# Kernel tuning notes

Hardware: AMD Instinct MI355X
Metric: run time of the kernel (lower is better)

## Reference

```python
import jax, jax.numpy as jnp
import numpy as np

H = 8   # no_heads
D = 32  # c_hidden per head


def setup_inputs() -> dict:
    key = jax.random.key(0)
    ks = jax.random.split(key, 8)
    B, Q, K, C = 4, 1024, 1024, 256
    s = 0.02
    return {
        "q_x": jax.random.normal(ks[0], (B, Q, C), jnp.float32),
        "kv_x": jax.random.normal(ks[1], (B, K, C), jnp.float32),
        "mask_bias": jnp.zeros((B, 1, 1, K), jnp.float32),
        "pair_bias": jax.random.normal(ks[2], (B, H, Q, K), jnp.float32),
        "wq": jax.random.normal(ks[3], (H * D, C), jnp.float32) * s,
        "wk": jax.random.normal(ks[4], (H * D, C), jnp.float32) * s,
        "wv": jax.random.normal(ks[5], (H * D, C), jnp.float32) * s,
        "wg": jax.random.normal(ks[6], (H * D, C), jnp.float32) * s,
        "bg": jnp.zeros((H * D,), jnp.float32),
        "wo": jax.random.normal(ks[7], (C, H * D), jnp.float32) * s,
        "bo": jnp.zeros((C,), jnp.float32),
    }


def reference(q_x, kv_x, mask_bias, pair_bias, wq, wk, wv, wg, bg, wo, bo):
    B, Q, _ = q_x.shape
    K = kv_x.shape[1]
    # linear projections (no bias on q/k/v, as in OpenFold Attention)
    q = (q_x @ wq.T).reshape(B, Q, H, D) / jnp.sqrt(jnp.asarray(D, q_x.dtype))
    k = (kv_x @ wk.T).reshape(B, K, H, D)
    v = (kv_x @ wv.T).reshape(B, K, H, D)
    # scores + biases (mask bias broadcasts over heads/queries)
    a = jnp.einsum("bqhd,bkhd->bhqk", q, k) + mask_bias + pair_bias
    a = jax.nn.softmax(a, axis=-1)
    o = jnp.einsum("bhqk,bkhd->bqhd", a, v)  # [B,Q,H,D]
    # multiplicative gating from the query input
    g = jax.nn.sigmoid(q_x @ wg.T + bg).reshape(B, Q, H, D)
    o = o * g
    return (o.reshape(B, Q, H * D)) @ wo.T + bo
```

## Files before the change

kernel.cpp:

```cpp
#include <hip/hip_runtime.h>
#include <cstdint>
#include <cstddef>

typedef short bf16x8 __attribute__((ext_vector_type(8)));
typedef float f32x4 __attribute__((ext_vector_type(4)));
typedef unsigned short u16x4 __attribute__((ext_vector_type(4)));
typedef unsigned short u16x8 __attribute__((ext_vector_type(8)));

#define MFMA(a,b,c) __builtin_amdgcn_mfma_f32_16x16x32_bf16((a),(b),(c),0,0,0)

__device__ __forceinline__ unsigned short f2bf(float x){
  union { float f; unsigned u; } v; v.f = x;
  unsigned r = v.u + 0x7FFFu + ((v.u >> 16) & 1u);
  return (unsigned short)(r >> 16);
}
__device__ __forceinline__ float bf2f(unsigned short b){
  union { unsigned u; float f; } v; v.u = ((unsigned)b) << 16;
  return v.f;
}
__device__ __forceinline__ bf16x8 cvtld8(const float* p){
  f32x4 a = *(const f32x4*)p;
  f32x4 b = *(const f32x4*)(p + 4);
  bf16x8 r;
  r[0]=(short)f2bf(a.x); r[1]=(short)f2bf(a.y);
  r[2]=(short)f2bf(a.z); r[3]=(short)f2bf(a.w);
  r[4]=(short)f2bf(b.x); r[5]=(short)f2bf(b.y);
  r[6]=(short)f2bf(b.z); r[7]=(short)f2bf(b.w);
  return r;
}

__global__ __launch_bounds__(256) void wcvt_kernel(
    const float* __restrict__ wq, const float* __restrict__ wk,
    const float* __restrict__ wv, const float* __restrict__ wg,
    const float* __restrict__ wo, unsigned short* __restrict__ dst)
{
  const int which = blockIdx.x >> 5;
  const float* s = (which==0)?wq:(which==1)?wk:(which==2)?wv:(which==3)?wg:wo;
  const int off = (blockIdx.x & 31) * 2048 + threadIdx.x * 8;
  f32x4 a = *(const f32x4*)(s + off);
  f32x4 b = *(const f32x4*)(s + off + 4);
  u16x8 r;
  r[0]=f2bf(a.x); r[1]=f2bf(a.y); r[2]=f2bf(a.z); r[3]=f2bf(a.w);
  r[4]=f2bf(b.x); r[5]=f2bf(b.y); r[6]=f2bf(b.z); r[7]=f2bf(b.w);
  *(u16x8*)(dst + (size_t)which*65536 + off) = r;
}

__global__ __launch_bounds__(256,2) void proj_kernel(
    const float* __restrict__ q_x, const float* __restrict__ kv_x,
    const unsigned short* __restrict__ wb,
    const float* __restrict__ bg,
    unsigned short* __restrict__ qws, unsigned short* __restrict__ kws,
    unsigned short* __restrict__ vTws, unsigned short* __restrict__ gws)
{
  const int tid = threadIdx.x;
  const int w = tid >> 6, lane = tid & 63;
  const int c = lane & 15, qd = lane >> 4;
  const int side = blockIdx.x >> 8;
  const int rb = (blockIdx.x & 255) * 16;
  const float* X = side ? kv_x : q_x;
  const unsigned short* W0 = wb + (size_t)(side ? 1 : 0) * 65536;
  const unsigned short* W1 = wb + (size_t)(side ? 2 : 3) * 65536;
  const int hdw = w * 64;

  const f32x4 fz = {0.f,0.f,0.f,0.f};
  f32x4 acc[2][4];
  #pragma unroll
  for (int o=0;o<2;o++)
    #pragma unroll
    for (int mt=0;mt<4;mt++) acc[o][mt] = fz;

  #pragma unroll
  for (int ks = 0; ks < 8; ks++){
    const int ko = ks*32 + qd*8;
    bf16x8 bfrag = cvtld8(X + (size_t)(rb + c)*256 + ko);
    #pragma unroll
    for (int mt = 0; mt < 4; mt++){
      const int hd = hdw + mt*16 + c;
      bf16x8 a0 = *(const bf16x8*)(W0 + (size_t)hd*256 + ko);
      bf16x8 a1 = *(const bf16x8*)(W1 + (size_t)hd*256 + ko);
      acc[0][mt] = MFMA(a0, bfrag, acc[0][mt]);
      acc[1][mt] = MFMA(a1, bfrag, acc[1][mt]);
    }
  }

  const int row = rb + c;
  const int b = row >> 10, rr = row & 1023;
  #pragma unroll
  for (int mt = 0; mt < 4; mt++){
    const int hd0 = hdw + mt*16 + qd*4;
    const int h = hd0 >> 5, d0 = hd0 & 31;
    f32x4 v0 = acc[0][mt], v1 = acc[1][mt];
    if (side == 0){
      const float qs = 0.17677669529663687f;
      u16x4 oq = { f2bf(v0.x*qs), f2bf(v0.y*qs), f2bf(v0.z*qs), f2bf(v0.w*qs) };
      *(u16x4*)(qws + ((size_t)((b*8 + h)*1024 + rr))*32 + d0) = oq;
      f32x4 bg4 = *(const f32x4*)(bg + hd0);
      float g0 = 1.f/(1.f + exp2f(-1.44269504f*(v1.x + bg4.x)));
      float g1 = 1.f/(1.f + exp2f(-1.44269504f*(v1.y + bg4.y)));
      float g2 = 1.f/(1.f + exp2f(-1.44269504f*(v1.z + bg4.z)));
      float g3 = 1.f/(1.f + exp2f(-1.44269504f*(v1.w + bg4.w)));
      u16x4 og = { f2bf(g0), f2bf(g1), f2bf(g2), f2bf(g3) };
      *(u16x4*)(gws + ((size_t)((b*1024 + rr)*8 + h))*32 + d0) = og;
    } else {
      u16x4 ok = { f2bf(v0.x), f2bf(v0.y), f2bf(v0.z), f2bf(v0.w) };
      *(u16x4*)(kws + ((size_t)((b*8 + h)*1024 + rr))*32 + d0) = ok;
      size_t vb = ((size_t)((b*8 + h)*32 + d0))*1024 + rr;
      vTws[vb         ] = f2bf(v1.x);
      vTws[vb + 1024  ] = f2bf(v1.y);
      vTws[vb + 2048  ] = f2bf(v1.z);
      vTws[vb + 3072  ] = f2bf(v1.w);
    }
  }
}

__global__ __launch_bounds__(256,2) void attn_kernel(
    const float* __restrict__ pair_bias, const float* __restrict__ mask_bias,
    const unsigned short* __restrict__ qws, const unsigned short* __restrict__ kws,
    const unsigned short* __restrict__ vTws, const unsigned short* __restrict__ gws,
    unsigned short* __restrict__ ows)
{
  __shared__ __align__(16) unsigned char smem[67072];
  unsigned short* kT = (unsigned short*)smem;
  unsigned short* vT = (unsigned short*)(smem + 16384);
  unsigned short* pT = (unsigned short*)(smem + 33280);

  const int tid = threadIdx.x;
  const int w = tid >> 6, lane = tid & 63;
  const int c = lane & 15, qd = lane >> 4;
  const int bh = blockIdx.x >> 4, qb = blockIdx.x & 15;
  const int b  = bh >> 3, h = bh & 7;
  const int qrow = qb*64 + w*16 + c;

  const bf16x8 qf = *(const bf16x8*)(qws + ((size_t)bh*1024 + qrow)*32 + qd*8);
  const float* pbp = pair_bias + ((size_t)bh*1024 + qrow)*1024;
  const float* mbp = mask_bias + (size_t)b*1024;
  unsigned short* pTw = pT + w*4224;

  const f32x4 fz = {0.f,0.f,0.f,0.f};
  float m_i = -3.0e38f, l_i = 0.f;
  f32x4 accO0 = fz, accO1 = fz;

  for (int kc = 0; kc < 4; kc++){
    const int k0 = kc*256;
    #pragma unroll
    for (int i = 0; i < 4; i++){
      const int idx = i*256 + tid;
      const int plane = idx >> 8, key = idx & 255;
      u16x8 t8 = *(const u16x8*)(kws + ((size_t)bh*1024 + k0 + key)*32 + plane*8);
      *(u16x8*)(kT + idx*8) = t8;
    }
    #pragma unroll
    for (int i = 0; i < 4; i++){
      const int idx = i*256 + tid;
      const int d = idx >> 5, kch = idx & 31;
      u16x8 t8 = *(const u16x8*)(vTws + ((size_t)bh*32 + d)*1024 + k0 + kch*8);
      *(u16x8*)(vT + d*264 + kch*8) = t8;
    }
    __syncthreads();

    f32x4 sf[16];
    float cmax = -3.0e38f;
    #pragma unroll
    for (int t = 0; t < 16; t++){
      bf16x8 af = *(const bf16x8*)(kT + (qd*256 + t*16 + c)*8);
      f32x4 s = MFMA(af, qf, fz);
      f32x4 pb = *(const f32x4*)(pbp + k0 + t*16 + qd*4);
      f32x4 mb = *(const f32x4*)(mbp + k0 + t*16 + qd*4);
      s = (s + pb + mb) * 1.44269504f;
      sf[t] = s;
      cmax = fmaxf(cmax, fmaxf(fmaxf(s.x, s.y), fmaxf(s.z, s.w)));
    }
    cmax = fmaxf(cmax, __shfl_xor(cmax, 16));
    cmax = fmaxf(cmax, __shfl_xor(cmax, 32));
    const float m_new = fmaxf(m_i, cmax);
    const float alpha = exp2f(m_i - m_new);
    accO0 *= alpha; accO1 *= alpha;

    float rsum = 0.f;
    #pragma unroll
    for (int t = 0; t < 16; t++){
      f32x4 p;
      p.x = exp2f(sf[t].x - m_new);
      p.y = exp2f(sf[t].y - m_new);
      p.z = exp2f(sf[t].z - m_new);
      p.w = exp2f(sf[t].w - m_new);
      rsum += (p.x + p.y) + (p.z + p.w);
      u16x4 pk = { f2bf(p.x), f2bf(p.y), f2bf(p.z), f2bf(p.w) };
      *(u16x4*)(pTw + c*264 + t*16 + qd*4) = pk;
    }
    rsum += __shfl_xor(rsum, 16);
    rsum += __shfl_xor(rsum, 32);
    l_i = l_i*alpha + rsum;
    m_i = m_new;

    #pragma unroll
    for (int ks = 0; ks < 8; ks++){
      bf16x8 pf = *(const bf16x8*)(pTw + c*264 + ks*32 + qd*8);
      bf16x8 v0 = *(const bf16x8*)(vT + c*264 + ks*32 + qd*8);
      bf16x8 v1 = *(const bf16x8*)(vT + (16 + c)*264 + ks*32 + qd*8);
      accO0 = MFMA(v0, pf, accO0);
      accO1 = MFMA(v1, pf, accO1);
    }
    __syncthreads();
  }

  const float inv_l = 1.0f / l_i;
  const size_t obase = (((size_t)b*1024 + qrow)*8 + h)*32;
  {
    u16x4 g4 = *(const u16x4*)(gws + obase + qd*4);
    u16x4 o4 = { f2bf(accO0.x*inv_l*bf2f(g4[0])),
                 f2bf(accO0.y*inv_l*bf2f(g4[1])),
                 f2bf(accO0.z*inv_l*bf2f(g4[2])),
                 f2bf(accO0.w*inv_l*bf2f(g4[3])) };
    *(u16x4*)(ows + obase + qd*4) = o4;
  }
  {
    u16x4 g4 = *(const u16x4*)(gws + obase + 16 + qd*4);
    u16x4 o4 = { f2bf(accO1.x*inv_l*bf2f(g4[0])),
                 f2bf(accO1.y*inv_l*bf2f(g4[1])),
                 f2bf(accO1.z*inv_l*bf2f(g4[2])),
                 f2bf(accO1.w*inv_l*bf2f(g4[3])) };
    *(u16x4*)(ows + obase + 16 + qd*4) = o4;
  }
}

__global__ __launch_bounds__(256,2) void oproj_kernel(
    const unsigned short* __restrict__ ows, const unsigned short* __restrict__ wob,
    const float* __restrict__ bo, float* __restrict__ out)
{
  const int tid = threadIdx.x;
  const int w = tid >> 6, lane = tid & 63;
  const int c = lane & 15, qd = lane >> 4;
  const int row0 = blockIdx.x * 16;
  const int i0 = w * 64;

  const f32x4 fz = {0.f,0.f,0.f,0.f};
  f32x4 acc[4] = {fz, fz, fz, fz};
  #pragma unroll
  for (int ks = 0; ks < 8; ks++){
    const int ko = ks*32 + qd*8;
    bf16x8 bfrag = *(const bf16x8*)(ows + (size_t)(row0 + c)*256 + ko);
    #pragma unroll
    for (int mt = 0; mt < 4; mt++){
      bf16x8 afrag = *(const bf16x8*)(wob + (size_t)(i0 + mt*16 + c)*256 + ko);
      acc[mt] = MFMA(afrag, bfrag, acc[mt]);
    }
  }
  #pragma unroll
  for (int mt = 0; mt < 4; mt++){
    const int i = i0 + mt*16 + qd*4;
    f32x4 bo4 = *(const f32x4*)(bo + i);
    f32x4 r = acc[mt] + bo4;
    *(f32x4*)(out + (size_t)(row0 + c)*256 + i) = r;
  }
}

extern "C" void kernel_launch(void* const* d_in, const int* in_sizes, int n_in,
                              void* d_out, int out_size, void* d_ws, size_t ws_size,
                              hipStream_t stream) {
  const float* q_x       = (const float*)d_in[0];
  const float* kv_x      = (const float*)d_in[1];
  const float* mask_bias = (const float*)d_in[2];
  const float* pair_bias = (const float*)d_in[3];
  const float* wq        = (const float*)d_in[4];
  const float* wk        = (const float*)d_in[5];
  const float* wv        = (const float*)d_in[6];
  const float* wg        = (const float*)d_in[7];
  const float* bg        = (const float*)d_in[8];
  const float* wo        = (const float*)d_in[9];
  const float* bo        = (const float*)d_in[10];

  unsigned short* ws  = (unsigned short*)d_ws;
  unsigned short* qws  = ws;
  unsigned short* kws  = ws + (1u<<20);
  unsigned short* vTws = ws + 2*(1u<<20);
  unsigned short* gws  = ws + 3*(1u<<20);
  unsigned short* ows  = ws + 4*(1u<<20);
  unsigned short* wb   = ws + 5*(1u<<20);

  wcvt_kernel<<<160, 256, 0, stream>>>(wq, wk, wv, wg, wo, wb);
  proj_kernel<<<512, 256, 0, stream>>>(q_x, kv_x, wb, bg, qws, kws, vTws, gws);
  attn_kernel<<<512, 256, 0, stream>>>(pair_bias, mask_bias, qws, kws, vTws, gws, ows);
  oproj_kernel<<<256, 256, 0, stream>>>(ows, wb + 4*65536, bo, (float*)d_out);
}
```

Baseline: 254.3 us.

## Read K/V fragments directly from global memory, drop LDS staging and block barriers

The attention kernel stops staging K and V^T tiles in shared memory and instead loads the MFMA operand fragments straight from global memory (relying on L1/L2 reuse across the four waves). The key chunk shrinks from 256 to 128, which shrinks the per-wave P buffer, and the two __syncthreads per chunk are removed. Launch bounds are raised to allow four blocks per SIMD group for higher occupancy. The trade-off is redundant global/L2 traffic for K/V, since each wave now fetches the same fragments, in exchange for less LDS use, no barriers, and more waves to hide the dominant pair_bias streaming latency.

Result: slower. 268.5 us (+5.6%).

```diff
diff --git a/kernel.cpp b/kernel.cpp
--- a/kernel.cpp
+++ b/kernel.cpp
@@ -113,16 +113,13 @@
   }
 }
 
-__global__ __launch_bounds__(256,2) void attn_kernel(
+__global__ __launch_bounds__(256,4) void attn_kernel(
     const float* __restrict__ pair_bias, const float* __restrict__ mask_bias,
     const unsigned short* __restrict__ qws, const unsigned short* __restrict__ kws,
     const unsigned short* __restrict__ vTws, const unsigned short* __restrict__ gws,
     unsigned short* __restrict__ ows)
 {
-  __shared__ __align__(16) unsigned char smem[67072];
-  unsigned short* kT = (unsigned short*)smem;
-  unsigned short* vT = (unsigned short*)(smem + 16384);
-  unsigned short* pT = (unsigned short*)(smem + 33280);
+  __shared__ __align__(16) unsigned short pT[4*16*136];
 
   const int tid = threadIdx.x;
   const int w = tid >> 6, lane = tid & 63;
@@ -134,38 +131,25 @@
   const bf16x8 qf = *(const bf16x8*)(qws + ((size_t)bh*1024 + qrow)*32 + qd*8);
   const float* pbp = pair_bias + ((size_t)bh*1024 + qrow)*1024;
   const float* mbp = mask_bias + (size_t)b*1024;
-  unsigned short* pTw = pT + w*4224;
+  const unsigned short* kbase = kws  + (size_t)bh*1024*32;
+  const unsigned short* vbase = vTws + (size_t)bh*32*1024;
+  unsigned short* pTw = pT + w*(16*136);
 
   const f32x4 fz = {0.f,0.f,0.f,0.f};
   float m_i = -3.0e38f, l_i = 0.f;
   f32x4 accO0 = fz, accO1 = fz;
 
-  for (int kc = 0; kc < 4; kc++){
-    const int k0 = kc*256;
-    #pragma unroll
-    for (int i = 0; i < 4; i++){
-      const int idx = i*256 + tid;
-      const int plane = idx >> 8, key = idx & 255;
-      u16x8 t8 = *(const u16x8*)(kws + ((size_t)bh*1024 + k0 + key)*32 + plane*8);
-      *(u16x8*)(kT + idx*8) = t8;
-    }
-    #pragma unroll
-    for (int i = 0; i < 4; i++){
-      const int idx = i*256 + tid;
-      const int d = idx >> 5, kch = idx & 31;
-      u16x8 t8 = *(const u16x8*)(vTws + ((size_t)bh*32 + d)*1024 + k0 + kch*8);
-      *(u16x8*)(vT + d*264 + kch*8) = t8;
-    }
-    __syncthreads();
-
-    f32x4 sf[16];
+  for (int kc = 0; kc < 8; kc++){
+    const int k0 = kc*128;
+    f32x4 sf[8];
     float cmax = -3.0e38f;
     #pragma unroll
-    for (int t = 0; t < 16; t++){
-      bf16x8 af = *(const bf16x8*)(kT + (qd*256 + t*16 + c)*8);
+    for (int t = 0; t < 8; t++){
+      const int kt = k0 + t*16;
+      bf16x8 af = *(const bf16x8*)(kbase + (size_t)(kt + c)*32 + qd*8);
       f32x4 s = MFMA(af, qf, fz);
-      f32x4 pb = *(const f32x4*)(pbp + k0 + t*16 + qd*4);
-      f32x4 mb = *(const f32x4*)(mbp + k0 + t*16 + qd*4);
+      f32x4 pb = *(const f32x4*)(pbp + kt + qd*4);
+      f32x4 mb = *(const f32x4*)(mbp + kt + qd*4);
       s = (s + pb + mb) * 1.44269504f;
       sf[t] = s;
       cmax = fmaxf(cmax, fmaxf(fmaxf(s.x, s.y), fmaxf(s.z, s.w)));
@@ -178,7 +162,7 @@
 
     float rsum = 0.f;
     #pragma unroll
-    for (int t = 0; t < 16; t++){
+    for (int t = 0; t < 8; t++){
       f32x4 p;
       p.x = exp2f(sf[t].x - m_new);
       p.y = exp2f(sf[t].y - m_new);
@@ -186,7 +170,7 @@
       p.w = exp2f(sf[t].w - m_new);
       rsum += (p.x + p.y) + (p.z + p.w);
       u16x4 pk = { f2bf(p.x), f2bf(p.y), f2bf(p.z), f2bf(p.w) };
-      *(u16x4*)(pTw + c*264 + t*16 + qd*4) = pk;
+      *(u16x4*)(pTw + c*136 + t*16 + qd*4) = pk;
     }
     rsum += __shfl_xor(rsum, 16);
     rsum += __shfl_xor(rsum, 32);
@@ -194,14 +178,13 @@
     m_i = m_new;
 
     #pragma unroll
-    for (int ks = 0; ks < 8; ks++){
-      bf16x8 pf = *(const bf16x8*)(pTw + c*264 + ks*32 + qd*8);
-      bf16x8 v0 = *(const bf16x8*)(vT + c*264 + ks*32 + qd*8);
-      bf16x8 v1 = *(const bf16x8*)(vT + (16 + c)*264 + ks*32 + qd*8);
+    for (int ks = 0; ks < 4; ks++){
+      bf16x8 pf = *(const bf16x8*)(pTw + c*136 + ks*32 + qd*8);
+      bf16x8 v0 = *(const bf16x8*)(vbase + (size_t)c*1024      + k0 + ks*32 + qd*8);
+      bf16x8 v1 = *(const bf16x8*)(vbase + (size_t)(16+c)*1024 + k0 + ks*32 + qd*8);
       accO0 = MFMA(v0, pf, accO0);
       accO1 = MFMA(v1, pf, accO1);
     }
-    __syncthreads();
   }
 
   const float inv_l = 1.0f / l_i;
```
